# Kernel optimization log

Hardware: AMD Instinct MI355X
Metric: run time of the kernel (lower is better)

The kernel has to match this reference:

```python
import jax, jax.numpy as jnp
import numpy as np

D_MODEL, N_STATE, L_MAX, BATCH = 512, 64, 2048, 8


def _make_dplr_hippo(n):
    # HiPPO-LegS -> NPLR -> DPLR (Annotated-S4 construction)
    p0 = np.sqrt(1.0 + 2.0 * np.arange(n))
    A = p0[:, None] * p0[None, :]
    A = -(np.tril(A) - np.diag(np.arange(n)))
    p = np.sqrt(np.arange(n) + 0.5)
    S = A + p[:, None] * p[None, :]          # normal part (skew-symmetric + const diag)
    lam_re = np.mean(np.diagonal(S)) * np.ones(n)
    lam_im, V = np.linalg.eigh(S * (-1j))
    p_rot = V.conj().T @ p
    return (lam_re.astype(np.float32), lam_im.astype(np.float32),
            p_rot.real.astype(np.float32), p_rot.imag.astype(np.float32))


def setup_inputs() -> dict:
    key = jax.random.key(0)
    k = jax.random.split(key, 8)
    lam_re, lam_im, p_re, p_im = _make_dplr_hippo(N_STATE)
    dt_min, dt_max = 1e-3, 1e-1
    log_step = (jax.random.uniform(k[0], (D_MODEL,))
                * (np.log(dt_max) - np.log(dt_min)) + np.log(dt_min)).astype(jnp.float32)
    s = 0.5 ** 0.5
    B_re = jax.random.normal(k[1], (D_MODEL, N_STATE), dtype=jnp.float32) * s
    B_im = jax.random.normal(k[2], (D_MODEL, N_STATE), dtype=jnp.float32) * s
    Ct_re = jax.random.normal(k[3], (D_MODEL, N_STATE), dtype=jnp.float32) * s
    Ct_im = jax.random.normal(k[4], (D_MODEL, N_STATE), dtype=jnp.float32) * s
    D = jnp.ones((D_MODEL,), jnp.float32)
    lim = 1.0 / np.sqrt(D_MODEL)
    W = jax.random.uniform(k[5], (D_MODEL, D_MODEL), minval=-lim, maxval=lim, dtype=jnp.float32)
    b = jax.random.uniform(k[6], (D_MODEL,), minval=-lim, maxval=lim, dtype=jnp.float32)
    u = jax.random.normal(k[7], (BATCH, L_MAX, D_MODEL), dtype=jnp.float32)
    return dict(u=u,
                lam_re=jnp.asarray(lam_re), lam_im=jnp.asarray(lam_im),
                p_re=jnp.asarray(p_re), p_im=jnp.asarray(p_im),
                B_re=B_re, B_im=B_im, Ct_re=Ct_re, Ct_im=Ct_im,
                log_step=log_step, D=D, W=W, b=b,
                ln_w=jnp.ones((D_MODEL,), jnp.float32),
                ln_b=jnp.zeros((D_MODEL,), jnp.float32))


def _s4_kernel(lam, p, Bc, Ct, step, L):
    # lam, p: (n,) complex; Bc, Ct: (H, n) complex; step: (H,)
    omega = jnp.exp((-2j * jnp.pi) * (jnp.arange(L) / L))          # (L,) roots of unity
    g = (2.0 / step[:, None]) * ((1.0 - omega) / (1.0 + omega))    # (H, L) bilinear transform
    c = 2.0 / (1.0 + omega)                                        # (L,)
    cauchy = 1.0 / (g[:, :, None] - lam)                           # (H, L, n)
    a0, a1 = Ct.conj(), jnp.conj(p)[None, :]
    b0, b1 = Bc, p[None, :]
    k00 = jnp.einsum('hn,hln->hl', a0 * b0, cauchy)
    k01 = jnp.einsum('hn,hln->hl', a0 * b1, cauchy)
    k10 = jnp.einsum('hn,hln->hl', a1 * b0, cauchy)
    k11 = jnp.einsum('hn,hln->hl', a1 * b1, cauchy)
    at_roots = c * (k00 - k01 * (1.0 / (1.0 + k11)) * k10)         # generating fn at roots
    return jnp.fft.ifft(at_roots, n=L, axis=-1).real               # (H, L) real SSM kernel


def reference(u, lam_re, lam_im, p_re, p_im, B_re, B_im, Ct_re, Ct_im,
              log_step, D, W, b, ln_w, ln_b):
    L = u.shape[1]
    lam = lam_re + 1j * lam_im
    p = p_re + 1j * p_im
    Bc = B_re + 1j * B_im
    Ct = Ct_re + 1j * Ct_im
    K = _s4_kernel(lam, p, Bc, Ct, jnp.exp(log_step), L)           # (H, L)
    # causal (non-circular) convolution via zero-padded FFT
    nfft = 2 * L
    Kf = jnp.fft.rfft(K, n=nfft, axis=-1)                          # (H, L+1)
    Uf = jnp.fft.rfft(u, n=nfft, axis=1)                           # (B, L+1, H)
    y = jnp.fft.irfft(Uf * Kf.T[None], n=nfft, axis=1)[:, :L]      # (B, L, H)
    y = y + D * u                                                  # skip connection
    z = jax.nn.gelu(y, approximate=False)                          # GELU (dropout p=0)
    z = jnp.einsum('blh,oh->blo', z, W) + b                        # Linear(d_model, d_model)
    r = z + u                                                      # residual
    mean = r.mean(-1, keepdims=True)
    var = r.var(-1, keepdims=True)
    return (r - mean) / jnp.sqrt(var + 1e-5) * ln_w + ln_b         # LayerNorm
```

## Files before the change

kernel.cpp:

```cpp
#include <hip/hip_runtime.h>
#include <hip/hip_bf16.h>
#include <math.h>

#define PI_F 3.14159265358979f

typedef __attribute__((ext_vector_type(8))) short bf16x8;
typedef __attribute__((ext_vector_type(4))) float f32x4;
typedef __attribute__((ext_vector_type(2))) float f32x2;

#define DM 512
#define LSEQ 2048
#define NB 8
#define NFFT 4096
#define MTOK (NB*LSEQ)

__device__ __forceinline__ float frcp(float x) { return __builtin_amdgcn_rcpf(x); }

__device__ __forceinline__ float gelu_fast(float y) {
  float t = 0.79788456f * (y + 0.044715f * y * y * y);
  float e = __expf(2.0f * t);
  float th = 1.0f - 2.0f * frcp(e + 1.0f);
  return 0.5f * y * (1.0f + th);
}

__device__ __forceinline__ int PD(int i) { return i + (i >> 5); }
#define LDSN 4224

template<bool INV>
__device__ __forceinline__ void dft8(const float xr[8], const float xi[8],
                                     float yr[8], float yi[8]) {
  const float C = 0.70710678118654752f;
  float t0r=xr[0]+xr[4], t0i=xi[0]+xi[4];
  float t1r=xr[0]-xr[4], t1i=xi[0]-xi[4];
  float t2r=xr[2]+xr[6], t2i=xi[2]+xi[6];
  float t3r=xr[2]-xr[6], t3i=xi[2]-xi[6];
  float it3r = INV ? -t3i : t3i;
  float it3i = INV ?  t3r : -t3r;
  float E0r=t0r+t2r, E0i=t0i+t2i;
  float E2r=t0r-t2r, E2i=t0i-t2i;
  float E1r=t1r+it3r, E1i=t1i+it3i;
  float E3r=t1r-it3r, E3i=t1i-it3i;
  float u0r=xr[1]+xr[5], u0i=xi[1]+xi[5];
  float u1r=xr[1]-xr[5], u1i=xi[1]-xi[5];
  float u2r=xr[3]+xr[7], u2i=xi[3]+xi[7];
  float u3r=xr[3]-xr[7], u3i=xi[3]-xi[7];
  float iu3r = INV ? -u3i : u3i;
  float iu3i = INV ?  u3r : -u3r;
  float O0r=u0r+u2r, O0i=u0i+u2i;
  float O2r=u0r-u2r, O2i=u0i-u2i;
  float O1r=u1r+iu3r, O1i=u1i+iu3i;
  float O3r=u1r-iu3r, O3i=u1i-iu3i;
  float w1r = INV ? C*(O1r-O1i) : C*(O1r+O1i);
  float w1i = INV ? C*(O1r+O1i) : C*(O1i-O1r);
  float w2r = INV ? -O2i : O2i;
  float w2i = INV ?  O2r : -O2r;
  float w3r = INV ? -C*(O3r+O3i) : C*(O3i-O3r);
  float w3i = INV ?  C*(O3r-O3i) : -C*(O3r+O3i);
  yr[0]=E0r+O0r; yi[0]=E0i+O0i;
  yr[4]=E0r-O0r; yi[4]=E0i-O0i;
  yr[1]=E1r+w1r; yi[1]=E1i+w1i;
  yr[5]=E1r-w1r; yi[5]=E1i-w1i;
  yr[2]=E2r+w2r; yi[2]=E2i+w2i;
  yr[6]=E2r-w2r; yi[6]=E2i-w2i;
  yr[3]=E3r+w3r; yi[3]=E3i+w3i;
  yr[7]=E3r-w3r; yi[7]=E3i-w3i;
}

template<bool INV>
__device__ __forceinline__ void dft16(const float xr[16], const float xi[16],
                                      float yr[16], float yi[16]) {
  float exr[8], exi[8], oxr[8], oxi[8];
  #pragma unroll
  for (int m = 0; m < 8; ++m) {
    exr[m]=xr[2*m];   exi[m]=xi[2*m];
    oxr[m]=xr[2*m+1]; oxi[m]=xi[2*m+1];
  }
  float er[8], ei[8], orr[8], oii[8];
  dft8<INV>(exr, exi, er, ei);
  dft8<INV>(oxr, oxi, orr, oii);
  const float KC = 0.92387953251128675f;
  const float KS = 0.38268343236508977f;
  const float KH = 0.70710678118654752f;
  float tr, ti;
  yr[0]=er[0]+orr[0]; yi[0]=ei[0]+oii[0];
  yr[8]=er[0]-orr[0]; yi[8]=ei[0]-oii[0];
  { float a=KC, b=INV?KS:-KS;
    tr=orr[1]*a-oii[1]*b; ti=orr[1]*b+oii[1]*a;
    yr[1]=er[1]+tr; yi[1]=ei[1]+ti; yr[9]=er[1]-tr; yi[9]=ei[1]-ti; }
  { float a=KH, b=INV?KH:-KH;
    tr=orr[2]*a-oii[2]*b; ti=orr[2]*b+oii[2]*a;
    yr[2]=er[2]+tr; yi[2]=ei[2]+ti; yr[10]=er[2]-tr; yi[10]=ei[2]-ti; }
  { float a=KS, b=INV?KC:-KC;
    tr=orr[3]*a-oii[3]*b; ti=orr[3]*b+oii[3]*a;
    yr[3]=er[3]+tr; yi[3]=ei[3]+ti; yr[11]=er[3]-tr; yi[11]=ei[3]-ti; }
  { if (INV) { tr=-oii[4]; ti= orr[4]; } else { tr= oii[4]; ti=-orr[4]; }
    yr[4]=er[4]+tr; yi[4]=ei[4]+ti; yr[12]=er[4]-tr; yi[12]=ei[4]-ti; }
  { float a=-KS, b=INV?KC:-KC;
    tr=orr[5]*a-oii[5]*b; ti=orr[5]*b+oii[5]*a;
    yr[5]=er[5]+tr; yi[5]=ei[5]+ti; yr[13]=er[5]-tr; yi[13]=ei[5]-ti; }
  { float a=-KH, b=INV?KH:-KH;
    tr=orr[6]*a-oii[6]*b; ti=orr[6]*b+oii[6]*a;
    yr[6]=er[6]+tr; yi[6]=ei[6]+ti; yr[14]=er[6]-tr; yi[14]=ei[6]-ti; }
  { float a=-KC, b=INV?KS:-KS;
    tr=orr[7]*a-oii[7]*b; ti=orr[7]*b+oii[7]*a;
    yr[7]=er[7]+tr; yi[7]=ei[7]+ti; yr[15]=er[7]-tr; yi[15]=ei[7]-ti; }
}

template<bool INV, int NSLOG, int NBF>
__device__ __forceinline__ void r16s(float* sr, float* si, int tid,
                                     float c1, float s1f) {
  float yr[16], yi[16];
  bool act = (NBF >= 256) || (tid < NBF);
  __syncthreads();
  if (act) {
    float xr[16], xi[16];
    #pragma unroll
    for (int m = 0; m < 16; ++m) {
      int ix = PD(tid + m * NBF);
      xr[m] = sr[ix]; xi[m] = si[ix];
    }
    if (NSLOG > 0) {
      float s1 = INV ? -s1f : s1f;
      float wr = c1, wi = s1;
      #pragma unroll
      for (int m = 1; m < 16; ++m) {
        float tr = xr[m]*wr - xi[m]*wi;
        float ti = xr[m]*wi + xi[m]*wr;
        xr[m] = tr; xi[m] = ti;
        float nr = wr*c1 - wi*s1;
        float ni = wr*s1 + wi*c1;
        wr = nr; wi = ni;
      }
    }
    dft16<INV>(xr, xi, yr, yi);
  }
  __syncthreads();
  if (act) {
    int r = tid & ((1 << NSLOG) - 1);
    int q = tid >> NSLOG;
    int base = (q << (NSLOG + 4)) + r;
    #pragma unroll
    for (int p = 0; p < 16; ++p) {
      int ix = PD(base + (p << NSLOG));
      sr[ix] = yr[p]; si[ix] = yi[p];
    }
  }
}

__device__ __forceinline__ void r16s_zfirst(float* sr, float* si, int tid) {
  const float KC = 0.92387953251128675f;
  const float KS = 0.38268343236508977f;
  const float KH = 0.70710678118654752f;
  float xr[8], xi[8];
  __syncthreads();
  #pragma unroll
  for (int m = 0; m < 8; ++m) {
    int ix = PD(tid + m * 256);
    xr[m] = sr[ix]; xi[m] = si[ix];
  }
  float er[8], ei[8];
  dft8<false>(xr, xi, er, ei);
  float tr[8], ti[8];
  tr[0] = xr[0];                      ti[0] = xi[0];
  tr[1] =  xr[1]*KC + xi[1]*KS;       ti[1] =  xi[1]*KC - xr[1]*KS;
  tr[2] = (xr[2] + xi[2])*KH;         ti[2] = (xi[2] - xr[2])*KH;
  tr[3] =  xr[3]*KS + xi[3]*KC;       ti[3] =  xi[3]*KS - xr[3]*KC;
  tr[4] =  xi[4];                     ti[4] = -xr[4];
  tr[5] = -xr[5]*KS + xi[5]*KC;       ti[5] = -xi[5]*KS - xr[5]*KC;
  tr[6] = (xi[6] - xr[6])*KH;         ti[6] = -(xr[6] + xi[6])*KH;
  tr[7] = -xr[7]*KC + xi[7]*KS;       ti[7] = -xi[7]*KC - xr[7]*KS;
  float odr[8], odi[8];
  dft8<false>(tr, ti, odr, odi);
  __syncthreads();
  int base = tid << 4;
  #pragma unroll
  for (int j = 0; j < 8; ++j) {
    int ie = PD(base + 2*j), io = PD(base + 2*j + 1);
    sr[ie] = er[j];  si[ie] = ei[j];
    sr[io] = odr[j]; si[io] = odi[j];
  }
}

template<bool INV, int NSLOG, int NBF>
__device__ __forceinline__ void r8s(float* sr, float* si, int tid,
                                    float c1, float s1f) {
  float yr[8], yi[8];
  bool act = (NBF >= 256) || (tid < NBF);
  __syncthreads();
  if (act) {
    float xr[8], xi[8];
    #pragma unroll
    for (int m = 0; m < 8; ++m) {
      int ix = PD(tid + m * NBF);
      xr[m] = sr[ix]; xi[m] = si[ix];
    }
    if (NSLOG > 0) {
      float s1 = INV ? -s1f : s1f;
      float wr = c1, wi = s1;
      #pragma unroll
      for (int m = 1; m < 8; ++m) {
        float tr = xr[m]*wr - xi[m]*wi;
        float ti = xr[m]*wi + xi[m]*wr;
        xr[m] = tr; xi[m] = ti;
        float nr = wr*c1 - wi*s1;
        float ni = wr*s1 + wi*c1;
        wr = nr; wi = ni;
      }
    }
    dft8<INV>(xr, xi, yr, yi);
  }
  __syncthreads();
  if (act) {
    int r = tid & ((1 << NSLOG) - 1);
    int q = tid >> NSLOG;
    int base = (q << (NSLOG + 3)) + r;
    #pragma unroll
    for (int p = 0; p < 8; ++p) {
      int ix = PD(base + (p << NSLOG));
      sr[ix] = yr[p]; si[ix] = yi[p];
    }
  }
}

template<bool INV>
__device__ __forceinline__ void fft4096(float* sr, float* si, int tid,
                                        float cA, float sA, float cB, float sB) {
  r16s<INV, 0, 256>(sr, si, tid, 1.f, 0.f);
  r16s<INV, 4, 256>(sr, si, tid, cA, sA);
  r16s<INV, 8, 256>(sr, si, tid, cB, sB);
  __syncthreads();
}

__device__ __forceinline__ void fft4096z(float* sr, float* si, int tid,
                                         float cA, float sA, float cB, float sB) {
  r16s_zfirst(sr, si, tid);
  r16s<false, 4, 256>(sr, si, tid, cA, sA);
  r16s<false, 8, 256>(sr, si, tid, cB, sB);
  __syncthreads();
}

template<bool INV>
__device__ __forceinline__ void fft2048(float* sr, float* si, int tid,
                                        float cA, float sA, float cB, float sB) {
  r8s <INV, 0, 256>(sr, si, tid, 1.f, 0.f);
  r16s<INV, 3, 128>(sr, si, tid, cA, sA);
  r16s<INV, 7, 128>(sr, si, tid, cB, sB);
  __syncthreads();
}

__global__ __launch_bounds__(256) void k_prep(
    const float* __restrict__ lam_re, const float* __restrict__ lam_im,
    const float* __restrict__ p_re,   const float* __restrict__ p_im,
    const float* __restrict__ B_re,   const float* __restrict__ B_im,
    const float* __restrict__ Ct_re,  const float* __restrict__ Ct_im,
    float* __restrict__ wtab,
    const float* __restrict__ W, __hip_bfloat16* __restrict__ Wb) {
  int bidx = blockIdx.x;
  if (bidx < 128) {
    int idx = bidx * 256 + threadIdx.x;
    int n = idx & 63;
    float br = B_re[idx],  bi = B_im[idx];
    float cr = Ct_re[idx], ci = Ct_im[idx];
    float pr = p_re[n],    pi = p_im[n];
    float* w = wtab + (size_t)idx * 12;
    w[0] = cr*br + ci*bi;   w[1] = cr*bi - ci*br;
    w[2] = cr*pr + ci*pi;   w[3] = cr*pi - ci*pr;
    w[4] = pr*br + pi*bi;   w[5] = pr*bi - pi*br;
    w[6] = pr*pr + pi*pi;   w[7] = lam_re[n];
    w[8] = lam_im[n];       w[9] = 0.f; w[10] = 0.f; w[11] = 0.f;
  } else {
    int i = (bidx - 128) * 256 + threadIdx.x;
    Wb[i] = __float2bfloat16(W[i]);
  }
}

__global__ __launch_bounds__(256) void k_cauchy(
    const float* __restrict__ wtab, const float* __restrict__ log_step,
    float2* __restrict__ atr) {
  int h = blockIdx.x >> 2;
  int l0 = ((blockIdx.x & 3) << 8) + threadIdx.x;
  int l1 = l0 + 1024;
  float two_over_step = 2.0f * expf(-log_step[h]);
  float omi0, omr0, omi1, omr1;
  sincosf(-2.0f * PI_F * (float)l0 / (float)LSEQ, &omi0, &omr0);
  sincosf(-2.0f * PI_F * (float)l1 / (float)LSEQ, &omi1, &omr1);
  float a0 = 1.0f + omr0, a1 = 1.0f + omr1;
  float iv0 = frcp(a0*a0 + omi0*omi0);
  float iv1 = frcp(a1*a1 + omi1*omi1);
  float cr0 = 2.0f*a0*iv0, ci0 = -2.0f*omi0*iv0;
  float cr1 = 2.0f*a1*iv1, ci1 = -2.0f*omi1*iv1;
  f32x2 gr, gi;
  gr.x = two_over_step * (1.0f - omr0*omr0 - omi0*omi0) * iv0;
  gr.y = two_over_step * (1.0f - omr1*omr1 - omi1*omi1) * iv1;
  gi.x = two_over_step * (-2.0f * omi0) * iv0;
  gi.y = two_over_step * (-2.0f * omi1) * iv1;
  f32x2 K00r={0.f,0.f},K00i={0.f,0.f},K01r={0.f,0.f},K01i={0.f,0.f},
        K10r={0.f,0.f},K10i={0.f,0.f},K11r={0.f,0.f},K11i={0.f,0.f};
  const float4* wq = (const float4*)(wtab + (size_t)h * 64 * 12);
  #pragma unroll 8
  for (int n = 0; n < 64; ++n) {
    float4 wa = wq[n*3+0];
    float4 wb = wq[n*3+1];
    float  lim = wq[n*3+2].x;
    f32x2 dr = gr - wb.w;
    f32x2 di = gi - lim;
    f32x2 den = dr*dr + di*di;
    f32x2 inv; inv.x = frcp(den.x); inv.y = frcp(den.y);
    f32x2 car = dr*inv, cai = -di*inv;
    K00r += wa.x*car - wa.y*cai;  K00i += wa.x*cai + wa.y*car;
    K01r += wa.z*car - wa.w*cai;  K01i += wa.z*cai + wa.w*car;
    K10r += wb.x*car - wb.y*cai;  K10i += wb.x*cai + wb.y*car;
    K11r += wb.z*car;             K11i += wb.z*cai;
  }
  {
    float tr = K01r.x*K10r.x - K01i.x*K10i.x, ti = K01r.x*K10i.x + K01i.x*K10r.x;
    float d1r = 1.0f + K11r.x, d1i = K11i.x;
    float invd1 = frcp(d1r*d1r + d1i*d1i);
    float t2r = (tr*d1r + ti*d1i) * invd1;
    float t2i = (ti*d1r - tr*d1i) * invd1;
    float numr = K00r.x - t2r, numi = K00i.x - t2i;
    atr[(size_t)h * LSEQ + l0] = make_float2(cr0*numr - ci0*numi, cr0*numi + ci0*numr);
  }
  {
    float tr = K01r.y*K10r.y - K01i.y*K10i.y, ti = K01r.y*K10i.y + K01i.y*K10r.y;
    float d1r = 1.0f + K11r.y, d1i = K11i.y;
    float invd1 = frcp(d1r*d1r + d1i*d1i);
    float t2r = (tr*d1r + ti*d1i) * invd1;
    float t2i = (ti*d1r - tr*d1i) * invd1;
    float numr = K00r.y - t2r, numi = K00i.y - t2i;
    atr[(size_t)h * LSEQ + l1] = make_float2(cr1*numr - ci1*numi, cr1*numi + ci1*numr);
  }
}

__global__ __launch_bounds__(256, 4) void k_fftK(const float2* __restrict__ atr,
                                                 float2* __restrict__ Kf) {
  __shared__ float sr[LDSN], si[LDSN];
  int h = blockIdx.x, tid = threadIdx.x;
  float c2a, s2a, c2b, s2b, c4a, s4a, c4b, s4b;
  { int r = tid & 7;   __sincosf(-2.f*PI_F*(float)r/128.f,  &s2a, &c2a); }
  { int r = tid & 127; __sincosf(-2.f*PI_F*(float)r/2048.f, &s2b, &c2b); }
  { int r = tid & 15;  __sincosf(-2.f*PI_F*(float)r/256.f,  &s4a, &c4a); }
  { int r = tid;       __sincosf(-2.f*PI_F*(float)r/4096.f, &s4b, &c4b); }
  const float2* ap = atr + (size_t)h * LSEQ;
  #pragma unroll
  for (int i = 0; i < 8; ++i) {
    int l = tid + i*256;
    float2 v = ap[l];
    sr[PD(l)] = v.x; si[PD(l)] = v.y;
  }
  fft2048<true>(sr, si, tid, c2a, s2a, c2b, s2b);
  #pragma unroll
  for (int i = 0; i < 8; ++i) {
    int m = tid + i*256;
    float v = sr[PD(m)] * (1.0f / (float)LSEQ);
    sr[PD(m)] = v;
    si[PD(m)] = 0.0f;
  }
  fft4096z(sr, si, tid, c4a, s4a, c4b, s4b);
  float2* ko = Kf + (size_t)h * NFFT;
  #pragma unroll
  for (int i = 0; i < 16; ++i) {
    int f = tid + i*256;
    ko[f] = make_float2(sr[PD(f)], si[PD(f)]);
  }
}

__global__ __launch_bounds__(256) void k_tr_u(const float* __restrict__ u,
                                              float* __restrict__ ut) {
  __shared__ float t[32][33];
  int b = blockIdx.z;
  int l0 = blockIdx.x * 32, h0 = blockIdx.y * 32;
  int x = threadIdx.x, y0 = threadIdx.y;
  #pragma unroll
  for (int i = 0; i < 4; ++i) {
    int y = y0 + i*8;
    t[y][x] = u[((size_t)b*LSEQ + l0 + y) * DM + h0 + x];
  }
  __syncthreads();
  #pragma unroll
  for (int i = 0; i < 4; ++i) {
    int y = y0 + i*8;
    ut[((size_t)b*DM + h0 + y) * LSEQ + l0 + x] = t[x][y];
  }
}

__global__ __launch_bounds__(256, 4) void k_conv(const float* __restrict__ ut,
                                                 const float2* __restrict__ Kf,
                                                 const float* __restrict__ Dvec,
                                                 __hip_bfloat16* __restrict__ zbt) {
  __shared__ float sr[LDSN], si[LDSN];
  int wg = blockIdx.x;
  int bp = wg >> 9, h = wg & 511;
  int b0 = bp*2, b1 = bp*2 + 1;
  int tid = threadIdx.x;
  float c4a, s4a, c4b, s4b;
  { int r = tid & 15; __sincosf(-2.f*PI_F*(float)r/256.f,  &s4a, &c4a); }
  { int r = tid;      __sincosf(-2.f*PI_F*(float)r/4096.f, &s4b, &c4b); }
  const float* u0p = ut + ((size_t)(b0*DM + h)) * LSEQ;
  const float* u1p = ut + ((size_t)(b1*DM + h)) * LSEQ;
  #pragma unroll
  for (int i = 0; i < 8; ++i) {
    int l = tid + i*256;
    sr[PD(l)] = u0p[l];  si[PD(l)] = u1p[l];
  }
  fft4096z(sr, si, tid, c4a, s4a, c4b, s4b);
  float yrg[16], yig[16];
  const float2* kp = Kf + (size_t)h * NFFT;
  #pragma unroll
  for (int i = 0; i < 16; ++i) {
    int f = tid + i*256;
    int fn = (NFFT - f) & (NFFT - 1);
    float ar = sr[PD(f)],  ai = si[PD(f)];
    float br = sr[PD(fn)], bi = -si[PD(fn)];
    float u0r = 0.5f*(ar + br), u0i = 0.5f*(ai + bi);
    float u1r = 0.5f*(ai - bi), u1i = -0.5f*(ar - br);
    float2 K0 = kp[f];
    float y0r = u0r*K0.x - u0i*K0.y, y0i = u0r*K0.y + u0i*K0.x;
    float y1r = u1r*K0.x - u1i*K0.y, y1i = u1r*K0.y + u1i*K0.x;
    yrg[i] = y0r - y1i;
    yig[i] = y0i + y1r;
  }
  __syncthreads();
  #pragma unroll
  for (int i = 0; i < 16; ++i) {
    int f = tid + i*256;
    sr[PD(f)] = yrg[i]; si[PD(f)] = yig[i];
  }
  fft4096<true>(sr, si, tid, c4a, s4a, c4b, s4b);
  float d = Dvec[h];
  __hip_bfloat16* zb0 = zbt + ((size_t)(b0*DM + h)) * LSEQ;
  __hip_bfloat16* zb1 = zbt + ((size_t)(b1*DM + h)) * LSEQ;
  const float inv_n = 1.0f / (float)NFFT;
  #pragma unroll
  for (int i = 0; i < 8; ++i) {
    int l = tid + i*256;
    float y0 = sr[PD(l)]*inv_n + d*u0p[l];
    float y1 = si[PD(l)]*inv_n + d*u1p[l];
    zb0[l] = __float2bfloat16(gelu_fast(y0));
    zb1[l] = __float2bfloat16(gelu_fast(y1));
  }
}

__global__ __launch_bounds__(256) void k_tr_z(const ushort* __restrict__ zt,
                                              ushort* __restrict__ Zb) {
  __shared__ ushort t[64][74];
  int b = blockIdx.z;
  int h0 = blockIdx.x * 64, l0 = blockIdx.y * 64;
  int x = threadIdx.x;
  int y = threadIdx.y;
  #pragma unroll
  for (int j = 0; j < 8; ++j) {
    int hh = y + j*8;
    uint v = *(const uint*)(zt + ((size_t)(b*DM + h0 + hh))*LSEQ + l0 + 2*x);
    *(uint*)&t[hh][2*x] = v;
  }
  __syncthreads();
  #pragma unroll
  for (int j = 0; j < 8; ++j) {
    int ll = y + j*8;
    uint lo = t[2*x][ll];
    uint hi = t[2*x+1][ll];
    uint v = lo | (hi << 16);
    *(uint*)(Zb + ((size_t)(b*LSEQ + l0 + ll))*DM + h0 + 2*x) = v;
  }
}

__global__ __launch_bounds__(512) void k_gemm_ln(
    const short* __restrict__ Z,
    const short* __restrict__ Wb,
    const float* __restrict__ bias,
    const float* __restrict__ u,
    const float* __restrict__ lnw, const float* __restrict__ lnb,
    float* __restrict__ out) {
  __shared__ short sA[32][40];
  __shared__ short sB[512][40];
  __shared__ float red[2][4][32];
  __shared__ float smu[32], srs[32];
  __shared__ float sln[2][DM];
  int tid = threadIdx.x, wave = tid >> 6, lane = tid & 63;
  int wm = wave >> 2, wn = wave & 3;
  int m0 = blockIdx.x * 32;
  int row = lane & 15, kq8 = (lane >> 4) << 3;
  sln[0][tid] = lnw[tid];
  sln[1][tid] = lnb[tid];
  f32x4 acc[8];
  #pragma unroll
  for (int j = 0; j < 8; ++j) acc[j] = (f32x4){0.f,0.f,0.f,0.f};
  for (int k0 = 0; k0 < DM; k0 += 32) {
    __syncthreads();
    if (tid < 128) {
      int srow = tid >> 2, skb = (tid & 3) << 3;
      *(uint4*)&sA[srow][skb] = *(const uint4*)(Z + (size_t)(m0 + srow)*DM + k0 + skb);
    }
    {
      int c = (tid & 3) << 3, r4 = tid >> 2;
      #pragma unroll
      for (int jj = 0; jj < 4; ++jj) {
        int o = r4 + jj*128;
        *(uint4*)&sB[o][c] = *(const uint4*)(Wb + (size_t)o*DM + k0 + c);
      }
    }
    __syncthreads();
    bf16x8 a0 = *(const bf16x8*)&sA[wm*16 + row][kq8];
    #pragma unroll
    for (int nt = 0; nt < 8; ++nt) {
      bf16x8 bf = *(const bf16x8*)&sB[wn*128 + nt*16 + row][kq8];
      acc[nt] = __builtin_amdgcn_mfma_f32_16x16x32_bf16(a0, bf, acc[nt], 0, 0, 0);
    }
  }
  int ccol = lane & 15, crow = (lane >> 4) << 2;
  #pragma unroll
  for (int rr = 0; rr < 4; ++rr) {
    int lr = wm*16 + crow + rr;
    int gr = m0 + lr;
    float ls = 0.f, ls2 = 0.f;
    #pragma unroll
    for (int nt = 0; nt < 8; ++nt) {
      int col = wn*128 + nt*16 + ccol;
      float v = acc[nt][rr] + bias[col] + u[(size_t)gr*DM + col];
      acc[nt][rr] = v;
      ls += v; ls2 += v*v;
    }
    ls  += __shfl_xor(ls, 1);  ls2 += __shfl_xor(ls2, 1);
    ls  += __shfl_xor(ls, 2);  ls2 += __shfl_xor(ls2, 2);
    ls  += __shfl_xor(ls, 4);  ls2 += __shfl_xor(ls2, 4);
    ls  += __shfl_xor(ls, 8);  ls2 += __shfl_xor(ls2, 8);
    if (ccol == 0) { red[0][wn][lr] = ls; red[1][wn][lr] = ls2; }
  }
  __syncthreads();
  if (tid < 32) {
    float s = red[0][0][tid] + red[0][1][tid] + red[0][2][tid] + red[0][3][tid];
    float q = red[1][0][tid] + red[1][1][tid] + red[1][2][tid] + red[1][3][tid];
    float mean = s * (1.0f/(float)DM);
    float var  = q * (1.0f/(float)DM) - mean*mean;
    smu[tid] = mean;
    srs[tid] = rsqrtf(var + 1e-5f);
  }
  __syncthreads();
  #pragma unroll
  for (int rr = 0; rr < 4; ++rr) {
    int lr = wm*16 + crow + rr;
    int gr = m0 + lr;
    float mu = smu[lr], rs = srs[lr];
    #pragma unroll
    for (int nt = 0; nt < 8; ++nt) {
      int col = wn*128 + nt*16 + ccol;
      out[(size_t)gr*DM + col] = (acc[nt][rr] - mu) * rs * sln[0][col] + sln[1][col];
    }
  }
}

extern "C" void kernel_launch(void* const* d_in, const int* in_sizes, int n_in,
                              void* d_out, int out_size, void* d_ws, size_t ws_size,
                              hipStream_t stream) {
  const float* u        = (const float*)d_in[0];
  const float* lam_re   = (const float*)d_in[1];
  const float* lam_im   = (const float*)d_in[2];
  const float* p_re     = (const float*)d_in[3];
  const float* p_im     = (const float*)d_in[4];
  const float* B_re     = (const float*)d_in[5];
  const float* B_im     = (const float*)d_in[6];
  const float* Ct_re    = (const float*)d_in[7];
  const float* Ct_im    = (const float*)d_in[8];
  const float* log_step = (const float*)d_in[9];
  const float* Dv       = (const float*)d_in[10];
  const float* W        = (const float*)d_in[11];
  const float* bias     = (const float*)d_in[12];
  const float* ln_w     = (const float*)d_in[13];
  const float* ln_b     = (const float*)d_in[14];
  float* out = (float*)d_out;
  char* ws = (char*)d_ws;

  float2* Kf = (float2*)ws;
  float*  ut = (float*)(ws + (16u << 20));
  __hip_bfloat16* zbt = (__hip_bfloat16*)(ws + (48u << 20));
  float2* atr  = (float2*)(ws + (48u << 20));
  float*  wtab = (float*)(ws + (56u << 20));
  __hip_bfloat16* Zb = (__hip_bfloat16*)(ws + (16u << 20));
  __hip_bfloat16* Wb = (__hip_bfloat16*)(ws + (64u << 20));
  if (ws_size < (65u << 20)) return;

  k_prep<<<dim3(128 + (DM*DM)/256), dim3(256), 0, stream>>>(
      lam_re, lam_im, p_re, p_im, B_re, B_im, Ct_re, Ct_im, wtab, W, Wb);
  k_cauchy<<<dim3(DM*4), dim3(256), 0, stream>>>(wtab, log_step, atr);
  k_fftK<<<dim3(DM), dim3(256), 0, stream>>>(atr, Kf);
  k_tr_u<<<dim3(LSEQ/32, DM/32, NB), dim3(32, 8), 0, stream>>>(u, ut);
  k_conv<<<dim3((NB/2) * DM), dim3(256), 0, stream>>>(ut, Kf, Dv, zbt);
  k_tr_z<<<dim3(DM/64, LSEQ/64, NB), dim3(32, 8), 0, stream>>>((const ushort*)zbt, (ushort*)Zb);
  k_gemm_ln<<<dim3(MTOK/32), dim3(512), 0, stream>>>((const short*)Zb, (const short*)Wb,
                                                     bias, u, ln_w, ln_b, out);
}
```

Baseline: 141.4 us.

## Fuse z transpose into GEMM load and merge Cauchy, u-transpose, W cast kernels

```diff
diff --git a/kernel.cpp b/kernel.cpp
--- a/kernel.cpp
+++ b/kernel.cpp
@@ -253,82 +253,101 @@
     const float* __restrict__ p_re,   const float* __restrict__ p_im,
     const float* __restrict__ B_re,   const float* __restrict__ B_im,
     const float* __restrict__ Ct_re,  const float* __restrict__ Ct_im,
-    float* __restrict__ wtab,
+    float* __restrict__ wtab) {
+  int idx = blockIdx.x * 256 + threadIdx.x;
+  int n = idx & 63;
+  float br = B_re[idx],  bi = B_im[idx];
+  float cr = Ct_re[idx], ci = Ct_im[idx];
+  float pr = p_re[n],    pi = p_im[n];
+  float* w = wtab + (size_t)idx * 12;
+  w[0] = cr*br + ci*bi;   w[1] = cr*bi - ci*br;
+  w[2] = cr*pr + ci*pi;   w[3] = cr*pi - ci*pr;
+  w[4] = pr*br + pi*bi;   w[5] = pr*bi - pi*br;
+  w[6] = pr*pr + pi*pi;   w[7] = lam_re[n];
+  w[8] = lam_im[n];       w[9] = 0.f; w[10] = 0.f; w[11] = 0.f;
+}
+
+__global__ __launch_bounds__(256) void k_mega(
+    const float* __restrict__ wtab, const float* __restrict__ log_step,
+    float2* __restrict__ atr,
+    const float* __restrict__ u, float* __restrict__ ut,
     const float* __restrict__ W, __hip_bfloat16* __restrict__ Wb) {
+  __shared__ float tsh[32][33];
   int bidx = blockIdx.x;
-  if (bidx < 128) {
-    int idx = bidx * 256 + threadIdx.x;
-    int n = idx & 63;
-    float br = B_re[idx],  bi = B_im[idx];
-    float cr = Ct_re[idx], ci = Ct_im[idx];
-    float pr = p_re[n],    pi = p_im[n];
-    float* w = wtab + (size_t)idx * 12;
-    w[0] = cr*br + ci*bi;   w[1] = cr*bi - ci*br;
-    w[2] = cr*pr + ci*pi;   w[3] = cr*pi - ci*pr;
-    w[4] = pr*br + pi*bi;   w[5] = pr*bi - pi*br;
-    w[6] = pr*pr + pi*pi;   w[7] = lam_re[n];
-    w[8] = lam_im[n];       w[9] = 0.f; w[10] = 0.f; w[11] = 0.f;
+  int tid = threadIdx.x;
+  if (bidx < 2048) {
+    int h = bidx >> 2;
+    int l0 = ((bidx & 3) << 8) + tid;
+    int l1 = l0 + 1024;
+    float two_over_step = 2.0f * expf(-log_step[h]);
+    float omi0, omr0, omi1, omr1;
+    sincosf(-2.0f * PI_F * (float)l0 / (float)LSEQ, &omi0, &omr0);
+    sincosf(-2.0f * PI_F * (float)l1 / (float)LSEQ, &omi1, &omr1);
+    float a0 = 1.0f + omr0, a1 = 1.0f + omr1;
+    float iv0 = frcp(a0*a0 + omi0*omi0);
+    float iv1 = frcp(a1*a1 + omi1*omi1);
+    float cr0 = 2.0f*a0*iv0, ci0 = -2.0f*omi0*iv0;
+    float cr1 = 2.0f*a1*iv1, ci1 = -2.0f*omi1*iv1;
+    f32x2 gr, gi;
+    gr.x = two_over_step * (1.0f - omr0*omr0 - omi0*omi0) * iv0;
+    gr.y = two_over_step * (1.0f - omr1*omr1 - omi1*omi1) * iv1;
+    gi.x = two_over_step * (-2.0f * omi0) * iv0;
+    gi.y = two_over_step * (-2.0f * omi1) * iv1;
+    f32x2 K00r={0.f,0.f},K00i={0.f,0.f},K01r={0.f,0.f},K01i={0.f,0.f},
+          K10r={0.f,0.f},K10i={0.f,0.f},K11r={0.f,0.f},K11i={0.f,0.f};
+    const float4* wq = (const float4*)(wtab + (size_t)h * 64 * 12);
+    #pragma unroll 8
+    for (int n = 0; n < 64; ++n) {
+      float4 wa = wq[n*3+0];
+      float4 wb = wq[n*3+1];
+      float  lim = wq[n*3+2].x;
+      f32x2 dr = gr - wb.w;
+      f32x2 di = gi - lim;
+      f32x2 den = dr*dr + di*di;
+      f32x2 inv; inv.x = frcp(den.x); inv.y = frcp(den.y);
+      f32x2 car = dr*inv, cai = -di*inv;
+      K00r += wa.x*car - wa.y*cai;  K00i += wa.x*cai + wa.y*car;
+      K01r += wa.z*car - wa.w*cai;  K01i += wa.z*cai + wa.w*car;
+      K10r += wb.x*car - wb.y*cai;  K10i += wb.x*cai + wb.y*car;
+      K11r += wb.z*car;             K11i += wb.z*cai;
+    }
+    {
+      float tr = K01r.x*K10r.x - K01i.x*K10i.x, ti = K01r.x*K10i.x + K01i.x*K10r.x;
+      float d1r = 1.0f + K11r.x, d1i = K11i.x;
+      float invd1 = frcp(d1r*d1r + d1i*d1i);
+      float t2r = (tr*d1r + ti*d1i) * invd1;
+      float t2i = (ti*d1r - tr*d1i) * invd1;
+      float numr = K00r.x - t2r, numi = K00i.x - t2i;
+      atr[(size_t)h * LSEQ + l0] = make_float2(cr0*numr - ci0*numi, cr0*numi + ci0*numr);
+    }
+    {
+      float tr = K01r.y*K10r.y - K01i.y*K10i.y, ti = K01r.y*K10i.y + K01i.y*K10r.y;
+      float d1r = 1.0f + K11r.y, d1i = K11i.y;
+      float invd1 = frcp(d1r*d1r + d1i*d1i);
+      float t2r = (tr*d1r + ti*d1i) * invd1;
+      float t2i = (ti*d1r - tr*d1i) * invd1;
+      float numr = K00r.y - t2r, numi = K00i.y - t2i;
+      atr[(size_t)h * LSEQ + l1] = make_float2(cr1*numr - ci1*numi, cr1*numi + ci1*numr);
+    }
+  } else if (bidx < 2048 + 8192) {
+    int t = bidx - 2048;
+    int lx = t & 63, hy = (t >> 6) & 15, b = t >> 10;
+    int l0 = lx * 32, h0 = hy * 32;
+    int x = tid & 31, y0 = tid >> 5;
+    #pragma unroll
+    for (int i = 0; i < 4; ++i) {
+      int y = y0 + i*8;
+      tsh[y][x] = u[((size_t)b*LSEQ + l0 + y) * DM + h0 + x];
+    }
+    __syncthreads();
+    #pragma unroll
+    for (int i = 0; i < 4; ++i) {
+      int y = y0 + i*8;
+      ut[((size_t)b*DM + h0 + y) * LSEQ + l0 + x] = tsh[x][y];
+    }
   } else {
-    int i = (bidx - 128) * 256 + threadIdx.x;
+    int i = (bidx - 10240) * 256 + tid;
     Wb[i] = __float2bfloat16(W[i]);
-  }
-}
-
-__global__ __launch_bounds__(256) void k_cauchy(
-    const float* __restrict__ wtab, const float* __restrict__ log_step,
-    float2* __restrict__ atr) {
-  int h = blockIdx.x >> 2;
-  int l0 = ((blockIdx.x & 3) << 8) + threadIdx.x;
-  int l1 = l0 + 1024;
-  float two_over_step = 2.0f * expf(-log_step[h]);
-  float omi0, omr0, omi1, omr1;
-  sincosf(-2.0f * PI_F * (float)l0 / (float)LSEQ, &omi0, &omr0);
-  sincosf(-2.0f * PI_F * (float)l1 / (float)LSEQ, &omi1, &omr1);
-  float a0 = 1.0f + omr0, a1 = 1.0f + omr1;
-  float iv0 = frcp(a0*a0 + omi0*omi0);
-  float iv1 = frcp(a1*a1 + omi1*omi1);
-  float cr0 = 2.0f*a0*iv0, ci0 = -2.0f*omi0*iv0;
-  float cr1 = 2.0f*a1*iv1, ci1 = -2.0f*omi1*iv1;
-  f32x2 gr, gi;
-  gr.x = two_over_step * (1.0f - omr0*omr0 - omi0*omi0) * iv0;
-  gr.y = two_over_step * (1.0f - omr1*omr1 - omi1*omi1) * iv1;
-  gi.x = two_over_step * (-2.0f * omi0) * iv0;
-  gi.y = two_over_step * (-2.0f * omi1) * iv1;
-  f32x2 K00r={0.f,0.f},K00i={0.f,0.f},K01r={0.f,0.f},K01i={0.f,0.f},
-        K10r={0.f,0.f},K10i={0.f,0.f},K11r={0.f,0.f},K11i={0.f,0.f};
-  const float4* wq = (const float4*)(wtab + (size_t)h * 64 * 12);
-  #pragma unroll 8
-  for (int n = 0; n < 64; ++n) {
-    float4 wa = wq[n*3+0];
-    float4 wb = wq[n*3+1];
-    float  lim = wq[n*3+2].x;
-    f32x2 dr = gr - wb.w;
-    f32x2 di = gi - lim;
-    f32x2 den = dr*dr + di*di;
-    f32x2 inv; inv.x = frcp(den.x); inv.y = frcp(den.y);
-    f32x2 car = dr*inv, cai = -di*inv;
-    K00r += wa.x*car - wa.y*cai;  K00i += wa.x*cai + wa.y*car;
-    K01r += wa.z*car - wa.w*cai;  K01i += wa.z*cai + wa.w*car;
-    K10r += wb.x*car - wb.y*cai;  K10i += wb.x*cai + wb.y*car;
-    K11r += wb.z*car;             K11i += wb.z*cai;
-  }
-  {
-    float tr = K01r.x*K10r.x - K01i.x*K10i.x, ti = K01r.x*K10i.x + K01i.x*K10r.x;
-    float d1r = 1.0f + K11r.x, d1i = K11i.x;
-    float invd1 = frcp(d1r*d1r + d1i*d1i);
-    float t2r = (tr*d1r + ti*d1i) * invd1;
-    float t2i = (ti*d1r - tr*d1i) * invd1;
-    float numr = K00r.x - t2r, numi = K00i.x - t2i;
-    atr[(size_t)h * LSEQ + l0] = make_float2(cr0*numr - ci0*numi, cr0*numi + ci0*numr);
-  }
-  {
-    float tr = K01r.y*K10r.y - K01i.y*K10i.y, ti = K01r.y*K10i.y + K01i.y*K10r.y;
-    float d1r = 1.0f + K11r.y, d1i = K11i.y;
-    float invd1 = frcp(d1r*d1r + d1i*d1i);
-    float t2r = (tr*d1r + ti*d1i) * invd1;
-    float t2i = (ti*d1r - tr*d1i) * invd1;
-    float numr = K00r.y - t2r, numi = K00i.y - t2i;
-    atr[(size_t)h * LSEQ + l1] = make_float2(cr1*numr - ci1*numi, cr1*numi + ci1*numr);
   }
 }
 
@@ -362,25 +381,6 @@
   for (int i = 0; i < 16; ++i) {
     int f = tid + i*256;
     ko[f] = make_float2(sr[PD(f)], si[PD(f)]);
-  }
-}
-
-__global__ __launch_bounds__(256) void k_tr_u(const float* __restrict__ u,
-                                              float* __restrict__ ut) {
-  __shared__ float t[32][33];
-  int b = blockIdx.z;
-  int l0 = blockIdx.x * 32, h0 = blockIdx.y * 32;
-  int x = threadIdx.x, y0 = threadIdx.y;
-  #pragma unroll
-  for (int i = 0; i < 4; ++i) {
-    int y = y0 + i*8;
-    t[y][x] = u[((size_t)b*LSEQ + l0 + y) * DM + h0 + x];
-  }
-  __syncthreads();
-  #pragma unroll
-  for (int i = 0; i < 4; ++i) {
-    int y = y0 + i*8;
-    ut[((size_t)b*DM + h0 + y) * LSEQ + l0 + x] = t[x][y];
   }
 }
 
@@ -441,94 +441,83 @@
   }
 }
 
-__global__ __launch_bounds__(256) void k_tr_z(const ushort* __restrict__ zt,
-                                              ushort* __restrict__ Zb) {
-  __shared__ ushort t[64][74];
-  int b = blockIdx.z;
-  int h0 = blockIdx.x * 64, l0 = blockIdx.y * 64;
-  int x = threadIdx.x;
-  int y = threadIdx.y;
-  #pragma unroll
-  for (int j = 0; j < 8; ++j) {
-    int hh = y + j*8;
-    uint v = *(const uint*)(zt + ((size_t)(b*DM + h0 + hh))*LSEQ + l0 + 2*x);
-    *(uint*)&t[hh][2*x] = v;
-  }
-  __syncthreads();
-  #pragma unroll
-  for (int j = 0; j < 8; ++j) {
-    int ll = y + j*8;
-    uint lo = t[2*x][ll];
-    uint hi = t[2*x+1][ll];
-    uint v = lo | (hi << 16);
-    *(uint*)(Zb + ((size_t)(b*LSEQ + l0 + ll))*DM + h0 + 2*x) = v;
-  }
-}
-
 __global__ __launch_bounds__(512) void k_gemm_ln(
-    const short* __restrict__ Z,
+    const ushort* __restrict__ zbt,
     const short* __restrict__ Wb,
     const float* __restrict__ bias,
     const float* __restrict__ u,
     const float* __restrict__ lnw, const float* __restrict__ lnb,
     float* __restrict__ out) {
-  __shared__ short sA[32][40];
+  __shared__ ushort sA[64][40];
   __shared__ short sB[512][40];
-  __shared__ float red[2][4][32];
-  __shared__ float smu[32], srs[32];
+  __shared__ float red[2][4][64];
+  __shared__ float smu[64], srs[64];
   __shared__ float sln[2][DM];
   int tid = threadIdx.x, wave = tid >> 6, lane = tid & 63;
   int wm = wave >> 2, wn = wave & 3;
-  int m0 = blockIdx.x * 32;
+  int m0 = blockIdx.x * 64;
+  int b = m0 >> 11;
+  int l0 = m0 & (LSEQ - 1);
+  const ushort* zb = zbt + (size_t)b * DM * LSEQ;
   int row = lane & 15, kq8 = (lane >> 4) << 3;
+  int kk = tid >> 4, seg = tid & 15;
+  int cB = (tid & 3) << 3, rB = tid >> 2;
   sln[0][tid] = lnw[tid];
   sln[1][tid] = lnb[tid];
-  f32x4 acc[8];
-  #pragma unroll
-  for (int j = 0; j < 8; ++j) acc[j] = (f32x4){0.f,0.f,0.f,0.f};
+  f32x4 acc[2][8];
+  #pragma unroll
+  for (int i = 0; i < 2; ++i)
+    #pragma unroll
+    for (int j = 0; j < 8; ++j) acc[i][j] = (f32x4){0.f,0.f,0.f,0.f};
   for (int k0 = 0; k0 < DM; k0 += 32) {
     __syncthreads();
-    if (tid < 128) {
-      int srow = tid >> 2, skb = (tid & 3) << 3;
-      *(uint4*)&sA[srow][skb] = *(const uint4*)(Z + (size_t)(m0 + srow)*DM + k0 + skb);
-    }
     {
-      int c = (tid & 3) << 3, r4 = tid >> 2;
-      #pragma unroll
-      for (int jj = 0; jj < 4; ++jj) {
-        int o = r4 + jj*128;
-        *(uint4*)&sB[o][c] = *(const uint4*)(Wb + (size_t)o*DM + k0 + c);
-      }
+      uint2 v = *(const uint2*)(zb + (size_t)(k0 + kk)*LSEQ + l0 + seg*4);
+      const ushort* p = (const ushort*)&v;
+      sA[seg*4 + 0][kk] = p[0];
+      sA[seg*4 + 1][kk] = p[1];
+      sA[seg*4 + 2][kk] = p[2];
+      sA[seg*4 + 3][kk] = p[3];
+    }
+    #pragma unroll
+    for (int jj = 0; jj < 4; ++jj) {
+      int o = rB + jj*128;
+      *(uint4*)&sB[o][cB] = *(const uint4*)(Wb + (size_t)o*DM + k0 + cB);
     }
     __syncthreads();
-    bf16x8 a0 = *(const bf16x8*)&sA[wm*16 + row][kq8];
+    bf16x8 a0 = *(const bf16x8*)&sA[wm*32 + row][kq8];
+    bf16x8 a1 = *(const bf16x8*)&sA[wm*32 + 16 + row][kq8];
     #pragma unroll
     for (int nt = 0; nt < 8; ++nt) {
       bf16x8 bf = *(const bf16x8*)&sB[wn*128 + nt*16 + row][kq8];
-      acc[nt] = __builtin_amdgcn_mfma_f32_16x16x32_bf16(a0, bf, acc[nt], 0, 0, 0);
+      acc[0][nt] = __builtin_amdgcn_mfma_f32_16x16x32_bf16(a0, bf, acc[0][nt], 0, 0, 0);
+      acc[1][nt] = __builtin_amdgcn_mfma_f32_16x16x32_bf16(a1, bf, acc[1][nt], 0, 0, 0);
     }
   }
   int ccol = lane & 15, crow = (lane >> 4) << 2;
   #pragma unroll
-  for (int rr = 0; rr < 4; ++rr) {
-    int lr = wm*16 + crow + rr;
-    int gr = m0 + lr;
-    float ls = 0.f, ls2 = 0.f;
-    #pragma unroll
-    for (int nt = 0; nt < 8; ++nt) {
-      int col = wn*128 + nt*16 + ccol;
-      float v = acc[nt][rr] + bias[col] + u[(size_t)gr*DM + col];
-      acc[nt][rr] = v;
-      ls += v; ls2 += v*v;
-    }
-    ls  += __shfl_xor(ls, 1);  ls2 += __shfl_xor(ls2, 1);
-    ls  += __shfl_xor(ls, 2);  ls2 += __shfl_xor(ls2, 2);
-    ls  += __shfl_xor(ls, 4);  ls2 += __shfl_xor(ls2, 4);
-    ls  += __shfl_xor(ls, 8);  ls2 += __shfl_xor(ls2, 8);
-    if (ccol == 0) { red[0][wn][lr] = ls; red[1][wn][lr] = ls2; }
-  }
-  __syncthreads();
-  if (tid < 32) {
+  for (int rt = 0; rt < 2; ++rt) {
+    #pragma unroll
+    for (int rr = 0; rr < 4; ++rr) {
+      int lr = wm*32 + rt*16 + crow + rr;
+      int gr = m0 + lr;
+      float ls = 0.f, ls2 = 0.f;
+      #pragma unroll
+      for (int nt = 0; nt < 8; ++nt) {
+        int col = wn*128 + nt*16 + ccol;
+        float v = acc[rt][nt][rr] + bias[col] + u[(size_t)gr*DM + col];
+        acc[rt][nt][rr] = v;
+        ls += v; ls2 += v*v;
+      }
+      ls  += __shfl_xor(ls, 1);  ls2 += __shfl_xor(ls2, 1);
+      ls  += __shfl_xor(ls, 2);  ls2 += __shfl_xor(ls2, 2);
+      ls  += __shfl_xor(ls, 4);  ls2 += __shfl_xor(ls2, 4);
+      ls  += __shfl_xor(ls, 8);  ls2 += __shfl_xor(ls2, 8);
+      if (ccol == 0) { red[0][wn][lr] = ls; red[1][wn][lr] = ls2; }
+    }
+  }
+  __syncthreads();
+  if (tid < 64) {
     float s = red[0][0][tid] + red[0][1][tid] + red[0][2][tid] + red[0][3][tid];
     float q = red[1][0][tid] + red[1][1][tid] + red[1][2][tid] + red[1][3][tid];
     float mean = s * (1.0f/(float)DM);
@@ -538,14 +527,17 @@
   }
   __syncthreads();
   #pragma unroll
-  for (int rr = 0; rr < 4; ++rr) {
-    int lr = wm*16 + crow + rr;
-    int gr = m0 + lr;
-    float mu = smu[lr], rs = srs[lr];
-    #pragma unroll
-    for (int nt = 0; nt < 8; ++nt) {
-      int col = wn*128 + nt*16 + ccol;
-      out[(size_t)gr*DM + col] = (acc[nt][rr] - mu) * rs * sln[0][col] + sln[1][col];
+  for (int rt = 0; rt < 2; ++rt) {
+    #pragma unroll
+    for (int rr = 0; rr < 4; ++rr) {
+      int lr = wm*32 + rt*16 + crow + rr;
+      int gr = m0 + lr;
+      float mu = smu[lr], rs = srs[lr];
+      #pragma unroll
+      for (int nt = 0; nt < 8; ++nt) {
+        int col = wn*128 + nt*16 + ccol;
+        out[(size_t)gr*DM + col] = (acc[rt][nt][rr] - mu) * rs * sln[0][col] + sln[1][col];
+      }
     }
   }
 }
@@ -576,17 +568,15 @@
   __hip_bfloat16* zbt = (__hip_bfloat16*)(ws + (48u << 20));
   float2* atr  = (float2*)(ws + (48u << 20));
   float*  wtab = (float*)(ws + (56u << 20));
-  __hip_bfloat16* Zb = (__hip_bfloat16*)(ws + (16u << 20));
   __hip_bfloat16* Wb = (__hip_bfloat16*)(ws + (64u << 20));
   if (ws_size < (65u << 20)) return;
 
-  k_prep<<<dim3(128 + (DM*DM)/256), dim3(256), 0, stream>>>(
-      lam_re, lam_im, p_re, p_im, B_re, B_im, Ct_re, Ct_im, wtab, W, Wb);
-  k_cauchy<<<dim3(DM*4), dim3(256), 0, stream>>>(wtab, log_step, atr);
+  k_prep<<<dim3(128), dim3(256), 0, stream>>>(lam_re, lam_im, p_re, p_im,
+                                              B_re, B_im, Ct_re, Ct_im, wtab);
+  k_mega<<<dim3(2048 + 8192 + 1024), dim3(256), 0, stream>>>(
+      wtab, log_step, atr, u, ut, W, Wb);
   k_fftK<<<dim3(DM), dim3(256), 0, stream>>>(atr, Kf);
-  k_tr_u<<<dim3(LSEQ/32, DM/32, NB), dim3(32, 8), 0, stream>>>(u, ut);
   k_conv<<<dim3((NB/2) * DM), dim3(256), 0, stream>>>(ut, Kf, Dv, zbt);
-  k_tr_z<<<dim3(DM/64, LSEQ/64, NB), dim3(32, 8), 0, stream>>>((const ushort*)zbt, (ushort*)Zb);
-  k_gemm_ln<<<dim3(MTOK/32), dim3(512), 0, stream>>>((const short*)Zb, (const short*)Wb,
+  k_gemm_ln<<<dim3(MTOK/64), dim3(512), 0, stream>>>((const ushort*)zbt, (const short*)Wb,
                                                      bias, u, ln_w, ln_b, out);
 }
```

New measurement: 125.7 us. -11.1%, faster.
